# Optimization experiments

Measured on AMD Instinct MI355X. Metric: run time of the kernel, lower is better.

Reference implementation:

```python
import jax, jax.numpy as jnp
import numpy as np

B, T, C = 4, 2048, 1024
N_HEAD = 16
HEAD_DIM = C // N_HEAD


def setup_inputs() -> dict:
    key = jax.random.key(0)
    ks = jax.random.split(key, 5)
    scale = 0.02
    return {
        "x": jax.random.normal(ks[0], (B, T, C), dtype=jnp.float32),
        "w_attn": jax.random.normal(ks[1], (C, 3 * C), dtype=jnp.float32) * scale,
        "b_attn": jax.random.normal(ks[2], (3 * C,), dtype=jnp.float32) * scale,
        "w_proj": jax.random.normal(ks[3], (C, C), dtype=jnp.float32) * scale,
        "b_proj": jax.random.normal(ks[4], (C,), dtype=jnp.float32) * scale,
    }


def reference(x, w_attn, b_attn, w_proj, b_proj):
    Bq, Tq, Cq = x.shape
    qkv = x @ w_attn + b_attn  # [B, T, 3C]
    q, k, v = jnp.split(qkv, 3, axis=2)
    # [B, H, T, D]
    q = q.reshape(Bq, Tq, N_HEAD, HEAD_DIM).transpose(0, 2, 1, 3)
    k = k.reshape(Bq, Tq, N_HEAD, HEAD_DIM).transpose(0, 2, 1, 3)
    v = v.reshape(Bq, Tq, N_HEAD, HEAD_DIM).transpose(0, 2, 1, 3)
    att = jnp.einsum("bhqd,bhkd->bhqk", q, k) * (HEAD_DIM ** -0.5)
    causal = jnp.tril(jnp.ones((Tq, Tq), dtype=bool))
    att = jnp.where(causal[None, None, :, :], att, -jnp.inf)
    att = jax.nn.softmax(att, axis=-1)
    out = jnp.einsum("bhqk,bhkd->bhqd", att, v)  # [B, H, T, D]
    out = out.transpose(0, 2, 1, 3).reshape(Bq, Tq, Cq)
    return out @ w_proj + b_proj
```

## Files before the change

kernel.cpp:

```cpp
#include <hip/hip_runtime.h>
#include <hip/hip_bf16.h>

#define Bsz 4
#define Tsz 2048
#define Csz 1024
#define NH  16
#define HD  64
#define NT  (Bsz * Tsz)

typedef unsigned short u16;
typedef unsigned int   u32;
typedef u16   u16x8  __attribute__((ext_vector_type(8)));
typedef u16   u16x4  __attribute__((ext_vector_type(4)));
typedef short s16x8  __attribute__((ext_vector_type(8)));
typedef float f32x4  __attribute__((ext_vector_type(4)));

__device__ __forceinline__ float b2f(u16 u) {
    union { unsigned int i; float f; } x; x.i = ((unsigned int)u) << 16; return x.f;
}
__device__ __forceinline__ u16 f2b(float f) {
    unsigned int u = __float_as_uint(f);
    return (u16)((u + 0x7FFF + ((u >> 16) & 1)) >> 16);
}
__device__ __forceinline__ float ex2(float x) {
    float r; asm("v_exp_f32 %0, %1" : "=v"(r) : "v"(x)); return r;
}

__global__ __launch_bounds__(256)
void conv_f32_bf16(const float* __restrict__ in, u16* __restrict__ out, int n8)
{
    int t = blockIdx.x * 256 + threadIdx.x;
    if (t >= n8) return;
    const float4* p = reinterpret_cast<const float4*>(in) + (size_t)t * 2;
    float4 a = p[0], b = p[1];
    u16x8 w;
    w[0] = f2b(a.x); w[1] = f2b(a.y); w[2] = f2b(a.z); w[3] = f2b(a.w);
    w[4] = f2b(b.x); w[5] = f2b(b.y); w[6] = f2b(b.z); w[7] = f2b(b.w);
    *(reinterpret_cast<u16x8*>(out) + t) = w;
}

__global__ __launch_bounds__(256)
void transpose_conv(const float* __restrict__ in, u16* __restrict__ out, int K, int N)
{
    __shared__ float tile[32][33];
    const int n0 = blockIdx.x * 32, k0 = blockIdx.y * 32;
    const int tx = threadIdx.x & 31, ty = threadIdx.x >> 5;
#pragma unroll
    for (int j = 0; j < 4; ++j)
        tile[ty + j * 8][tx] = in[(size_t)(k0 + ty + j * 8) * N + n0 + tx];
    __syncthreads();
#pragma unroll
    for (int j = 0; j < 4; ++j)
        out[(size_t)(n0 + ty + j * 8) * K + k0 + tx] = f2b(tile[tx][ty + j * 8]);
}

template<typename OutT>
__global__ __launch_bounds__(256)
void gemm_bf16(const u16* __restrict__ A, const u16* __restrict__ Bt,
               const float* __restrict__ bias, OutT* __restrict__ C,
               int M, int N, int K)
{
    __shared__ u16 As[128 * 64];
    __shared__ u16 Bs[128 * 64];

    const int tid  = threadIdx.x;
    const int lane = tid & 63;
    const int wid  = tid >> 6;
    const int wr   = wid >> 1;
    const int wc   = wid & 1;
    const int g    = lane >> 4;
    const int rr   = lane & 15;

    const int n0 = blockIdx.x * 128;
    const int m0 = blockIdx.y * 128;

    f32x4 acc[4][4];
#pragma unroll
    for (int m = 0; m < 4; ++m)
#pragma unroll
        for (int n = 0; n < 4; ++n) acc[m][n] = (f32x4){0.f, 0.f, 0.f, 0.f};

    for (int k0 = 0; k0 < K; k0 += 64) {
        s16x8 va[4], vb[4];
#pragma unroll
        for (int p = 0; p < 4; ++p) {
            const int ci = p * 256 + tid;
            const int r = ci >> 3, s = ci & 7;
            va[p] = *reinterpret_cast<const s16x8*>(A  + (size_t)(m0 + r) * K + k0 + s * 8);
            vb[p] = *reinterpret_cast<const s16x8*>(Bt + (size_t)(n0 + r) * K + k0 + s * 8);
        }
        __syncthreads();
#pragma unroll
        for (int p = 0; p < 4; ++p) {
            const int ci = p * 256 + tid;
            const int r = ci >> 3, s = ci & 7;
            const int phys = r * 64 + ((s ^ (r & 7)) * 8);
            *reinterpret_cast<s16x8*>(&As[phys]) = va[p];
            *reinterpret_cast<s16x8*>(&Bs[phys]) = vb[p];
        }
        __syncthreads();

#pragma unroll
        for (int kk = 0; kk < 2; ++kk) {
            s16x8 af[4], bfr[4];
            const int s = kk * 4 + g;
#pragma unroll
            for (int m = 0; m < 4; ++m) {
                const int r = wr * 64 + m * 16 + rr;
                af[m] = *reinterpret_cast<const s16x8*>(&As[r * 64 + ((s ^ (r & 7)) * 8)]);
            }
#pragma unroll
            for (int n = 0; n < 4; ++n) {
                const int r = wc * 64 + n * 16 + rr;
                bfr[n] = *reinterpret_cast<const s16x8*>(&Bs[r * 64 + ((s ^ (r & 7)) * 8)]);
            }
#pragma unroll
            for (int m = 0; m < 4; ++m)
#pragma unroll
                for (int n = 0; n < 4; ++n)
                    acc[m][n] = __builtin_amdgcn_mfma_f32_16x16x32_bf16(
                        af[m], bfr[n], acc[m][n], 0, 0, 0);
        }
    }

#pragma unroll
    for (int m = 0; m < 4; ++m) {
#pragma unroll
        for (int n = 0; n < 4; ++n) {
            const int col = n0 + wc * 64 + n * 16 + rr;
            const float bv = bias[col];
#pragma unroll
            for (int j = 0; j < 4; ++j) {
                const int row = m0 + wr * 64 + m * 16 + g * 4 + j;
                const float v = acc[m][n][j] + bv;
                if constexpr (sizeof(OutT) == 2)
                    C[(size_t)row * N + col] = (OutT)f2b(v);
                else
                    C[(size_t)row * N + col] = (OutT)v;
            }
        }
    }
}

__global__ __launch_bounds__(256)
void attn_mfma(const u16* __restrict__ qkv, u16* __restrict__ out)
{
    __shared__ __align__(128) u16 Ks[64 * 64];
    __shared__ __align__(128) u16 Vt[64 * 64];
    __shared__ __align__(128) u16 Pl[4 * 2048];

    const int tid  = threadIdx.x;
    const int lane = tid & 63;
    const int wid  = tid >> 6;
    const int c    = lane & 15;
    const int g    = lane >> 4;

    const int bh = blockIdx.x;
    const int b  = bh >> 4;
    const int h  = bh & 15;
    const int t0 = ((int)gridDim.y - 1 - (int)blockIdx.y) * 128;
    const int qb0 = t0 + wid * 32;

    s16x8 qf[2][2];
#pragma unroll
    for (int m = 0; m < 2; ++m)
#pragma unroll
        for (int kk = 0; kk < 2; ++kk)
            qf[m][kk] = *reinterpret_cast<const s16x8*>(
                qkv + (size_t)(b * Tsz + qb0 + m * 16 + c) * (3 * Csz) + h * HD + kk * 32 + g * 8);

    f32x4 acco[2][4];
#pragma unroll
    for (int m = 0; m < 2; ++m)
#pragma unroll
        for (int dn = 0; dn < 4; ++dn) acco[m][dn] = (f32x4){0.f, 0.f, 0.f, 0.f};
    float mrun[8], lrun[8];
#pragma unroll
    for (int i = 0; i < 8; ++i) { mrun[i] = -1e30f; lrun[i] = 0.f; }

    const int skey = tid >> 3;
    const int sb   = tid & 7;
    const u32 pbyte = ((u32)(size_t)(&Pl[0])) + wid * 4096 + lane * 8;
    const float SC = 0.18033688f;

    for (int kt = 0; kt < t0 + 128; kt += 64) {
#pragma unroll
        for (int p = 0; p < 2; ++p) {
            const int key = skey + p * 32;
            const u16* gk = qkv + (size_t)(b * Tsz + kt + key) * (3 * Csz) + Csz + h * HD + sb * 8;
            u16x8 kv = *reinterpret_cast<const u16x8*>(gk);
            u16x8 vv = *reinterpret_cast<const u16x8*>(gk + Csz);
            *reinterpret_cast<u16x8*>(&Ks[key * 64 + ((sb ^ (key & 7)) * 8)]) = kv;
#pragma unroll
            for (int i = 0; i < 8; ++i) {
                const int d = sb * 8 + i;
                Vt[d * 64 + (key ^ (((i ^ sb) & 7) << 3))] = vv[i];
            }
        }
        __syncthreads();

        if (kt <= qb0 + 31) {
            f32x4 accS[2][4];
#pragma unroll
            for (int m = 0; m < 2; ++m)
#pragma unroll
                for (int n = 0; n < 4; ++n) accS[m][n] = (f32x4){0.f, 0.f, 0.f, 0.f};
#pragma unroll
            for (int kk = 0; kk < 2; ++kk) {
                s16x8 kf[4];
#pragma unroll
                for (int n = 0; n < 4; ++n) {
                    const int key = n * 16 + c;
                    kf[n] = *reinterpret_cast<const s16x8*>(
                        &Ks[key * 64 + (((kk * 4 + g) ^ (c & 7)) * 8)]);
                }
#pragma unroll
                for (int m = 0; m < 2; ++m)
#pragma unroll
                    for (int n = 0; n < 4; ++n)
                        accS[m][n] = __builtin_amdgcn_mfma_f32_16x16x32_bf16(
                            qf[m][kk], kf[n], accS[m][n], 0, 0, 0);
            }

            if (kt + 63 > qb0) {
#pragma unroll
                for (int m = 0; m < 2; ++m)
#pragma unroll
                    for (int n = 0; n < 4; ++n) {
                        const int kgl = kt + n * 16 + c;
#pragma unroll
                        for (int j = 0; j < 4; ++j) {
                            const int qg = qb0 + m * 16 + g * 4 + j;
                            if (kgl > qg) accS[m][n][j] = -1e30f;
                        }
                    }
            }

            float pm[8];
#pragma unroll
            for (int m = 0; m < 2; ++m)
#pragma unroll
                for (int j = 0; j < 4; ++j)
                    pm[m * 4 + j] = fmaxf(fmaxf(accS[m][0][j], accS[m][1][j]),
                                          fmaxf(accS[m][2][j], accS[m][3][j]));
#pragma unroll
            for (int msk = 1; msk < 16; msk <<= 1)
#pragma unroll
                for (int i = 0; i < 8; ++i)
                    pm[i] = fmaxf(pm[i], __shfl_xor(pm[i], msk));
            float cvec[8];
#pragma unroll
            for (int i = 0; i < 8; ++i) {
                const float mn = fmaxf(mrun[i], pm[i]);
                cvec[i] = ex2((mrun[i] - mn) * SC);
                mrun[i] = mn;
                lrun[i] *= cvec[i];
            }
#pragma unroll
            for (int m = 0; m < 2; ++m)
#pragma unroll
                for (int dn = 0; dn < 4; ++dn)
#pragma unroll
                    for (int j = 0; j < 4; ++j)
                        acco[m][dn][j] *= cvec[m * 4 + j];

#pragma unroll
            for (int m = 0; m < 2; ++m)
#pragma unroll
                for (int n = 0; n < 4; ++n) {
                    u16x4 pb;
#pragma unroll
                    for (int j = 0; j < 4; ++j) {
                        const float p = ex2((accS[m][n][j] - mrun[m * 4 + j]) * SC);
                        lrun[m * 4 + j] += p;
                        pb[j] = f2b(p);
                    }
                    const int slot = (n >> 1) * 32 + ((c >> 2) & 1) * 16
                                   + ((n & 1) * 2 + (c >> 3)) * 4 + (c & 3);
                    *reinterpret_cast<u16x4*>(&Pl[wid * 2048 + m * 1024 + slot * 16 + g * 4]) = pb;
                }
            asm volatile("s_waitcnt lgkmcnt(0)" ::: "memory");
            __builtin_amdgcn_sched_barrier(0);

            u16x4 t000, t001, t010, t011, t100, t101, t110, t111;
            asm volatile("ds_read_b64_tr_b16 %0, %1"             : "=v"(t000) : "v"(pbyte));
            asm volatile("ds_read_b64_tr_b16 %0, %1 offset:512"  : "=v"(t001) : "v"(pbyte));
            asm volatile("ds_read_b64_tr_b16 %0, %1 offset:1024" : "=v"(t010) : "v"(pbyte));
            asm volatile("ds_read_b64_tr_b16 %0, %1 offset:1536" : "=v"(t011) : "v"(pbyte));
            asm volatile("ds_read_b64_tr_b16 %0, %1 offset:2048" : "=v"(t100) : "v"(pbyte));
            asm volatile("ds_read_b64_tr_b16 %0, %1 offset:2560" : "=v"(t101) : "v"(pbyte));
            asm volatile("ds_read_b64_tr_b16 %0, %1 offset:3072" : "=v"(t110) : "v"(pbyte));
            asm volatile("ds_read_b64_tr_b16 %0, %1 offset:3584" : "=v"(t111) : "v"(pbyte));
            asm volatile("s_waitcnt lgkmcnt(0)" ::: "memory");
            __builtin_amdgcn_sched_barrier(0);

            s16x8 pa[2][2];
#pragma unroll
            for (int q = 0; q < 4; ++q) {
                pa[0][0][q] = (short)t000[q]; pa[0][0][q + 4] = (short)t001[q];
                pa[0][1][q] = (short)t010[q]; pa[0][1][q + 4] = (short)t011[q];
                pa[1][0][q] = (short)t100[q]; pa[1][0][q + 4] = (short)t101[q];
                pa[1][1][q] = (short)t110[q]; pa[1][1][q + 4] = (short)t111[q];
            }

#pragma unroll
            for (int kk = 0; kk < 2; ++kk) {
                s16x8 vf[4];
#pragma unroll
                for (int dn = 0; dn < 4; ++dn) {
                    const int d = dn * 16 + c;
                    const int swz = (c & 7) ^ ((dn * 2 + (c >> 3)) & 7);
                    vf[dn] = *reinterpret_cast<const s16x8*>(
                        &Vt[d * 64 + (((kk * 4 + g) ^ swz) * 8)]);
                }
#pragma unroll
                for (int m = 0; m < 2; ++m)
#pragma unroll
                    for (int dn = 0; dn < 4; ++dn)
                        acco[m][dn] = __builtin_amdgcn_mfma_f32_16x16x32_bf16(
                            pa[m][kk], vf[dn], acco[m][dn], 0, 0, 0);
            }
        }
        __syncthreads();
    }

#pragma unroll
    for (int msk = 1; msk < 16; msk <<= 1)
#pragma unroll
        for (int i = 0; i < 8; ++i)
            lrun[i] += __shfl_xor(lrun[i], msk);
    float inv[8];
#pragma unroll
    for (int i = 0; i < 8; ++i) inv[i] = 1.f / lrun[i];
#pragma unroll
    for (int m = 0; m < 2; ++m)
#pragma unroll
        for (int dn = 0; dn < 4; ++dn)
#pragma unroll
            for (int j = 0; j < 4; ++j) {
                const int q = qb0 + m * 16 + g * 4 + j;
                out[(size_t)(b * Tsz + q) * Csz + h * HD + dn * 16 + c] =
                    f2b(acco[m][dn][j] * inv[m * 4 + j]);
            }
}

extern "C" void kernel_launch(void* const* d_in, const int* in_sizes, int n_in,
                              void* d_out, int out_size, void* d_ws, size_t ws_size,
                              hipStream_t stream) {
    const float* x      = (const float*)d_in[0];
    const float* w_attn = (const float*)d_in[1];
    const float* b_attn = (const float*)d_in[2];
    const float* w_proj = (const float*)d_in[3];
    const float* b_proj = (const float*)d_in[4];
    float* out = (float*)d_out;

    char* w = (char*)d_ws;
    u16* qkv_bf = (u16*)w;  w += (size_t)NT * 3 * Csz * 2;
    u16* x_bf   = (u16*)w;  w += (size_t)NT * Csz * 2;
    u16* ao_bf  = (u16*)w;  w += (size_t)NT * Csz * 2;
    u16* wat    = (u16*)w;  w += (size_t)3 * Csz * Csz * 2;
    u16* wpt    = (u16*)w;

    conv_f32_bf16<<<(NT * Csz / 8 + 255) / 256, 256, 0, stream>>>(x, x_bf, NT * Csz / 8);
    transpose_conv<<<dim3(3 * Csz / 32, Csz / 32), 256, 0, stream>>>(w_attn, wat, Csz, 3 * Csz);
    transpose_conv<<<dim3(Csz / 32, Csz / 32), 256, 0, stream>>>(w_proj, wpt, Csz, Csz);

    gemm_bf16<u16><<<dim3(3 * Csz / 128, NT / 128), 256, 0, stream>>>(
        x_bf, wat, b_attn, qkv_bf, NT, 3 * Csz, Csz);

    attn_mfma<<<dim3(Bsz * NH, Tsz / 128), 256, 0, stream>>>(qkv_bf, ao_bf);

    gemm_bf16<float><<<dim3(Csz / 128, NT / 128), 256, 0, stream>>>(
        ao_bf, wpt, b_proj, out, NT, Csz, Csz);
}
```

Baseline: 306.6 us.

## Use direct global-to-LDS loads in GEMM and pair causal query tiles in attention

The GEMM now stages A and B tiles with global_load_lds straight into LDS instead of going through registers, which also drops the XOR swizzle (risking bank conflicts on the fragment reads). The attention kernel pairs query tile y with tile 15-y in each block to balance causal work, and halves the grid. It also folds the softmax scale into Q up front, skips rescaling the running max unless the max grows by more than a threshold (lazy rescale), and packs P to bf16 with v_cvt_pk_bf16_f32. Pre-scaling Q in bf16 adds a small rounding change, and the smaller grid may lower occupancy.

```diff
diff --git a/kernel.cpp b/kernel.cpp
--- a/kernel.cpp
+++ b/kernel.cpp
@@ -12,6 +12,7 @@
 typedef unsigned int   u32;
 typedef u16   u16x8  __attribute__((ext_vector_type(8)));
 typedef u16   u16x4  __attribute__((ext_vector_type(4)));
+typedef u32   u32x2  __attribute__((ext_vector_type(2)));
 typedef short s16x8  __attribute__((ext_vector_type(8)));
 typedef float f32x4  __attribute__((ext_vector_type(4)));
 
@@ -24,6 +25,14 @@
 }
 __device__ __forceinline__ float ex2(float x) {
     float r; asm("v_exp_f32 %0, %1" : "=v"(r) : "v"(x)); return r;
+}
+__device__ __forceinline__ u32 cvtpk(float lo, float hi) {
+    u32 r; asm("v_cvt_pk_bf16_f32 %0, %1, %2" : "=v"(r) : "v"(lo), "v"(hi)); return r;
+}
+__device__ __forceinline__ void gload16(const u16* g, u16* l) {
+    __builtin_amdgcn_global_load_lds(
+        (const __attribute__((address_space(1))) void*)g,
+        (__attribute__((address_space(3))) void*)l, 16, 0, 0);
 }
 
 __global__ __launch_bounds__(256)
@@ -70,6 +79,8 @@
     const int wc   = wid & 1;
     const int g    = lane >> 4;
     const int rr   = lane & 15;
+    const int srow = lane >> 3;
+    const int sslt = lane & 7;
 
     const int n0 = blockIdx.x * 128;
     const int m0 = blockIdx.y * 128;
@@ -81,22 +92,13 @@
         for (int n = 0; n < 4; ++n) acc[m][n] = (f32x4){0.f, 0.f, 0.f, 0.f};
 
     for (int k0 = 0; k0 < K; k0 += 64) {
-        s16x8 va[4], vb[4];
+        __syncthreads();
 #pragma unroll
         for (int p = 0; p < 4; ++p) {
-            const int ci = p * 256 + tid;
-            const int r = ci >> 3, s = ci & 7;
-            va[p] = *reinterpret_cast<const s16x8*>(A  + (size_t)(m0 + r) * K + k0 + s * 8);
-            vb[p] = *reinterpret_cast<const s16x8*>(Bt + (size_t)(n0 + r) * K + k0 + s * 8);
-        }
-        __syncthreads();
-#pragma unroll
-        for (int p = 0; p < 4; ++p) {
-            const int ci = p * 256 + tid;
-            const int r = ci >> 3, s = ci & 7;
-            const int phys = r * 64 + ((s ^ (r & 7)) * 8);
-            *reinterpret_cast<s16x8*>(&As[phys]) = va[p];
-            *reinterpret_cast<s16x8*>(&Bs[phys]) = vb[p];
+            const int q = p * 4 + wid;
+            const int r = q * 8 + srow;
+            gload16(A  + (size_t)(m0 + r) * K + k0 + sslt * 8, &As[q * 512]);
+            gload16(Bt + (size_t)(n0 + r) * K + k0 + sslt * 8, &Bs[q * 512]);
         }
         __syncthreads();
 
@@ -105,15 +107,13 @@
             s16x8 af[4], bfr[4];
             const int s = kk * 4 + g;
 #pragma unroll
-            for (int m = 0; m < 4; ++m) {
-                const int r = wr * 64 + m * 16 + rr;
-                af[m] = *reinterpret_cast<const s16x8*>(&As[r * 64 + ((s ^ (r & 7)) * 8)]);
-            }
-#pragma unroll
-            for (int n = 0; n < 4; ++n) {
-                const int r = wc * 64 + n * 16 + rr;
-                bfr[n] = *reinterpret_cast<const s16x8*>(&Bs[r * 64 + ((s ^ (r & 7)) * 8)]);
-            }
+            for (int m = 0; m < 4; ++m)
+                af[m] = *reinterpret_cast<const s16x8*>(
+                    &As[(wr * 64 + m * 16 + rr) * 64 + s * 8]);
+#pragma unroll
+            for (int n = 0; n < 4; ++n)
+                bfr[n] = *reinterpret_cast<const s16x8*>(
+                    &Bs[(wc * 64 + n * 16 + rr) * 64 + s * 8]);
 #pragma unroll
             for (int m = 0; m < 4; ++m)
 #pragma unroll
@@ -158,190 +158,208 @@
     const int bh = blockIdx.x;
     const int b  = bh >> 4;
     const int h  = bh & 15;
-    const int t0 = ((int)gridDim.y - 1 - (int)blockIdx.y) * 128;
-    const int qb0 = t0 + wid * 32;
-
-    s16x8 qf[2][2];
-#pragma unroll
-    for (int m = 0; m < 2; ++m)
-#pragma unroll
-        for (int kk = 0; kk < 2; ++kk)
-            qf[m][kk] = *reinterpret_cast<const s16x8*>(
-                qkv + (size_t)(b * Tsz + qb0 + m * 16 + c) * (3 * Csz) + h * HD + kk * 32 + g * 8);
-
-    f32x4 acco[2][4];
-#pragma unroll
-    for (int m = 0; m < 2; ++m)
-#pragma unroll
-        for (int dn = 0; dn < 4; ++dn) acco[m][dn] = (f32x4){0.f, 0.f, 0.f, 0.f};
-    float mrun[8], lrun[8];
-#pragma unroll
-    for (int i = 0; i < 8; ++i) { mrun[i] = -1e30f; lrun[i] = 0.f; }
-
     const int skey = tid >> 3;
     const int sb   = tid & 7;
     const u32 pbyte = ((u32)(size_t)(&Pl[0])) + wid * 4096 + lane * 8;
-    const float SC = 0.18033688f;
-
-    for (int kt = 0; kt < t0 + 128; kt += 64) {
-#pragma unroll
-        for (int p = 0; p < 2; ++p) {
-            const int key = skey + p * 32;
-            const u16* gk = qkv + (size_t)(b * Tsz + kt + key) * (3 * Csz) + Csz + h * HD + sb * 8;
-            u16x8 kv = *reinterpret_cast<const u16x8*>(gk);
-            u16x8 vv = *reinterpret_cast<const u16x8*>(gk + Csz);
-            *reinterpret_cast<u16x8*>(&Ks[key * 64 + ((sb ^ (key & 7)) * 8)]) = kv;
-#pragma unroll
-            for (int i = 0; i < 8; ++i) {
-                const int d = sb * 8 + i;
-                Vt[d * 64 + (key ^ (((i ^ sb) & 7) << 3))] = vv[i];
+    const float QSC = 0.18033688f;
+
+    for (int half = 0; half < 2; ++half) {
+        const int yt = half ? 15 - (int)blockIdx.y : (int)blockIdx.y;
+        const int t0 = yt * 128;
+        const int qb0 = t0 + wid * 32;
+
+        s16x8 qf[2][2];
+#pragma unroll
+        for (int m = 0; m < 2; ++m)
+#pragma unroll
+            for (int kk = 0; kk < 2; ++kk) {
+                u16x8 raw = *reinterpret_cast<const u16x8*>(
+                    qkv + (size_t)(b * Tsz + qb0 + m * 16 + c) * (3 * Csz)
+                        + h * HD + kk * 32 + g * 8);
+                s16x8 qv;
+#pragma unroll
+                for (int i = 0; i < 8; ++i) qv[i] = (short)f2b(b2f(raw[i]) * QSC);
+                qf[m][kk] = qv;
             }
+
+        f32x4 acco[2][4];
+#pragma unroll
+        for (int m = 0; m < 2; ++m)
+#pragma unroll
+            for (int dn = 0; dn < 4; ++dn) acco[m][dn] = (f32x4){0.f, 0.f, 0.f, 0.f};
+        float mrun[8], lrun[8];
+#pragma unroll
+        for (int i = 0; i < 8; ++i) { mrun[i] = -1e30f; lrun[i] = 0.f; }
+
+        for (int kt = 0; kt < t0 + 128; kt += 64) {
+#pragma unroll
+            for (int p = 0; p < 2; ++p) {
+                const int key = skey + p * 32;
+                const u16* gk = qkv + (size_t)(b * Tsz + kt + key) * (3 * Csz)
+                                + Csz + h * HD + sb * 8;
+                u16x8 kv = *reinterpret_cast<const u16x8*>(gk);
+                u16x8 vv = *reinterpret_cast<const u16x8*>(gk + Csz);
+                *reinterpret_cast<u16x8*>(&Ks[key * 64 + ((sb ^ (key & 7)) * 8)]) = kv;
+#pragma unroll
+                for (int i = 0; i < 8; ++i) {
+                    const int d = sb * 8 + i;
+                    Vt[d * 64 + (key ^ (((i ^ sb) & 7) << 3))] = vv[i];
+                }
+            }
+            __syncthreads();
+
+            if (kt <= qb0 + 31) {
+                f32x4 accS[2][4];
+#pragma unroll
+                for (int m = 0; m < 2; ++m)
+#pragma unroll
+                    for (int n = 0; n < 4; ++n) accS[m][n] = (f32x4){0.f, 0.f, 0.f, 0.f};
+#pragma unroll
+                for (int kk = 0; kk < 2; ++kk) {
+                    s16x8 kf[4];
+#pragma unroll
+                    for (int n = 0; n < 4; ++n) {
+                        const int key = n * 16 + c;
+                        kf[n] = *reinterpret_cast<const s16x8*>(
+                            &Ks[key * 64 + (((kk * 4 + g) ^ (c & 7)) * 8)]);
+                    }
+#pragma unroll
+                    for (int m = 0; m < 2; ++m)
+#pragma unroll
+                        for (int n = 0; n < 4; ++n)
+                            accS[m][n] = __builtin_amdgcn_mfma_f32_16x16x32_bf16(
+                                qf[m][kk], kf[n], accS[m][n], 0, 0, 0);
+                }
+
+                if (kt + 63 > qb0) {
+#pragma unroll
+                    for (int m = 0; m < 2; ++m)
+#pragma unroll
+                        for (int n = 0; n < 4; ++n) {
+                            const int kgl = kt + n * 16 + c;
+#pragma unroll
+                            for (int j = 0; j < 4; ++j) {
+                                const int qg = qb0 + m * 16 + g * 4 + j;
+                                if (kgl > qg) accS[m][n][j] = -1e30f;
+                            }
+                        }
+                }
+
+                float pm[8];
+#pragma unroll
+                for (int m = 0; m < 2; ++m)
+#pragma unroll
+                    for (int j = 0; j < 4; ++j)
+                        pm[m * 4 + j] = fmaxf(fmaxf(accS[m][0][j], accS[m][1][j]),
+                                              fmaxf(accS[m][2][j], accS[m][3][j]));
+#pragma unroll
+                for (int msk = 1; msk < 16; msk <<= 1)
+#pragma unroll
+                    for (int i = 0; i < 8; ++i)
+                        pm[i] = fmaxf(pm[i], __shfl_xor(pm[i], msk));
+
+                int need = 0;
+#pragma unroll
+                for (int i = 0; i < 8; ++i) need |= (pm[i] > mrun[i] + 8.f);
+                if (__any(need)) {
+                    float cvec[8];
+#pragma unroll
+                    for (int i = 0; i < 8; ++i) {
+                        const float mn = fmaxf(mrun[i], pm[i]);
+                        cvec[i] = ex2(mrun[i] - mn);
+                        mrun[i] = mn;
+                        lrun[i] *= cvec[i];
+                    }
+#pragma unroll
+                    for (int m = 0; m < 2; ++m)
+#pragma unroll
+                        for (int dn = 0; dn < 4; ++dn)
+#pragma unroll
+                            for (int j = 0; j < 4; ++j)
+                                acco[m][dn][j] *= cvec[m * 4 + j];
+                }
+
+#pragma unroll
+                for (int m = 0; m < 2; ++m)
+#pragma unroll
+                    for (int n = 0; n < 4; ++n) {
+                        float pv[4];
+#pragma unroll
+                        for (int j = 0; j < 4; ++j) {
+                            pv[j] = ex2(accS[m][n][j] - mrun[m * 4 + j]);
+                            lrun[m * 4 + j] += pv[j];
+                        }
+                        const u32 w0 = cvtpk(pv[0], pv[1]);
+                        const u32 w1 = cvtpk(pv[2], pv[3]);
+                        const int slot = (n >> 1) * 32 + ((c >> 2) & 1) * 16
+                                       + ((n & 1) * 2 + (c >> 3)) * 4 + (c & 3);
+                        *reinterpret_cast<u32x2*>(
+                            &Pl[wid * 2048 + m * 1024 + slot * 16 + g * 4]) = (u32x2){w0, w1};
+                    }
+                asm volatile("s_waitcnt lgkmcnt(0)" ::: "memory");
+                __builtin_amdgcn_sched_barrier(0);
+
+                u16x4 t000, t001, t010, t011, t100, t101, t110, t111;
+                asm volatile("ds_read_b64_tr_b16 %0, %1"             : "=v"(t000) : "v"(pbyte));
+                asm volatile("ds_read_b64_tr_b16 %0, %1 offset:512"  : "=v"(t001) : "v"(pbyte));
+                asm volatile("ds_read_b64_tr_b16 %0, %1 offset:1024" : "=v"(t010) : "v"(pbyte));
+                asm volatile("ds_read_b64_tr_b16 %0, %1 offset:1536" : "=v"(t011) : "v"(pbyte));
+                asm volatile("ds_read_b64_tr_b16 %0, %1 offset:2048" : "=v"(t100) : "v"(pbyte));
+                asm volatile("ds_read_b64_tr_b16 %0, %1 offset:2560" : "=v"(t101) : "v"(pbyte));
+                asm volatile("ds_read_b64_tr_b16 %0, %1 offset:3072" : "=v"(t110) : "v"(pbyte));
+                asm volatile("ds_read_b64_tr_b16 %0, %1 offset:3584" : "=v"(t111) : "v"(pbyte));
+                asm volatile("s_waitcnt lgkmcnt(0)" ::: "memory");
+                __builtin_amdgcn_sched_barrier(0);
+
+                s16x8 pa[2][2];
+#pragma unroll
+                for (int q = 0; q < 4; ++q) {
+                    pa[0][0][q] = (short)t000[q]; pa[0][0][q + 4] = (short)t001[q];
+                    pa[0][1][q] = (short)t010[q]; pa[0][1][q + 4] = (short)t011[q];
+                    pa[1][0][q] = (short)t100[q]; pa[1][0][q + 4] = (short)t101[q];
+                    pa[1][1][q] = (short)t110[q]; pa[1][1][q + 4] = (short)t111[q];
+                }
+
+#pragma unroll
+                for (int kk = 0; kk < 2; ++kk) {
+                    s16x8 vf[4];
+#pragma unroll
+                    for (int dn = 0; dn < 4; ++dn) {
+                        const int d = dn * 16 + c;
+                        const int swz = (c & 7) ^ ((dn * 2 + (c >> 3)) & 7);
+                        vf[dn] = *reinterpret_cast<const s16x8*>(
+                            &Vt[d * 64 + (((kk * 4 + g) ^ swz) * 8)]);
+                    }
+#pragma unroll
+                    for (int m = 0; m < 2; ++m)
+#pragma unroll
+                        for (int dn = 0; dn < 4; ++dn)
+                            acco[m][dn] = __builtin_amdgcn_mfma_f32_16x16x32_bf16(
+                                pa[m][kk], vf[dn], acco[m][dn], 0, 0, 0);
+                }
+            }
+            __syncthreads();
         }
-        __syncthreads();
-
-        if (kt <= qb0 + 31) {
-            f32x4 accS[2][4];
-#pragma unroll
-            for (int m = 0; m < 2; ++m)
-#pragma unroll
-                for (int n = 0; n < 4; ++n) accS[m][n] = (f32x4){0.f, 0.f, 0.f, 0.f};
-#pragma unroll
-            for (int kk = 0; kk < 2; ++kk) {
-                s16x8 kf[4];
-#pragma unroll
-                for (int n = 0; n < 4; ++n) {
-                    const int key = n * 16 + c;
-                    kf[n] = *reinterpret_cast<const s16x8*>(
-                        &Ks[key * 64 + (((kk * 4 + g) ^ (c & 7)) * 8)]);
-                }
-#pragma unroll
-                for (int m = 0; m < 2; ++m)
-#pragma unroll
-                    for (int n = 0; n < 4; ++n)
-                        accS[m][n] = __builtin_amdgcn_mfma_f32_16x16x32_bf16(
-                            qf[m][kk], kf[n], accS[m][n], 0, 0, 0);
-            }
-
-            if (kt + 63 > qb0) {
-#pragma unroll
-                for (int m = 0; m < 2; ++m)
-#pragma unroll
-                    for (int n = 0; n < 4; ++n) {
-                        const int kgl = kt + n * 16 + c;
-#pragma unroll
-                        for (int j = 0; j < 4; ++j) {
-                            const int qg = qb0 + m * 16 + g * 4 + j;
-                            if (kgl > qg) accS[m][n][j] = -1e30f;
-                        }
-                    }
-            }
-
-            float pm[8];
-#pragma unroll
-            for (int m = 0; m < 2; ++m)
-#pragma unroll
-                for (int j = 0; j < 4; ++j)
-                    pm[m * 4 + j] = fmaxf(fmaxf(accS[m][0][j], accS[m][1][j]),
-                                          fmaxf(accS[m][2][j], accS[m][3][j]));
-#pragma unroll
-            for (int msk = 1; msk < 16; msk <<= 1)
-#pragma unroll
-                for (int i = 0; i < 8; ++i)
-                    pm[i] = fmaxf(pm[i], __shfl_xor(pm[i], msk));
-            float cvec[8];
-#pragma unroll
-            for (int i = 0; i < 8; ++i) {
-                const float mn = fmaxf(mrun[i], pm[i]);
-                cvec[i] = ex2((mrun[i] - mn) * SC);
-                mrun[i] = mn;
-                lrun[i] *= cvec[i];
-            }
-#pragma unroll
-            for (int m = 0; m < 2; ++m)
-#pragma unroll
-                for (int dn = 0; dn < 4; ++dn)
-#pragma unroll
-                    for (int j = 0; j < 4; ++j)
-                        acco[m][dn][j] *= cvec[m * 4 + j];
-
-#pragma unroll
-            for (int m = 0; m < 2; ++m)
-#pragma unroll
-                for (int n = 0; n < 4; ++n) {
-                    u16x4 pb;
-#pragma unroll
-                    for (int j = 0; j < 4; ++j) {
-                        const float p = ex2((accS[m][n][j] - mrun[m * 4 + j]) * SC);
-                        lrun[m * 4 + j] += p;
-                        pb[j] = f2b(p);
-                    }
-                    const int slot = (n >> 1) * 32 + ((c >> 2) & 1) * 16
-                                   + ((n & 1) * 2 + (c >> 3)) * 4 + (c & 3);
-                    *reinterpret_cast<u16x4*>(&Pl[wid * 2048 + m * 1024 + slot * 16 + g * 4]) = pb;
-                }
-            asm volatile("s_waitcnt lgkmcnt(0)" ::: "memory");
-            __builtin_amdgcn_sched_barrier(0);
-
-            u16x4 t000, t001, t010, t011, t100, t101, t110, t111;
-            asm volatile("ds_read_b64_tr_b16 %0, %1"             : "=v"(t000) : "v"(pbyte));
-            asm volatile("ds_read_b64_tr_b16 %0, %1 offset:512"  : "=v"(t001) : "v"(pbyte));
-            asm volatile("ds_read_b64_tr_b16 %0, %1 offset:1024" : "=v"(t010) : "v"(pbyte));
-            asm volatile("ds_read_b64_tr_b16 %0, %1 offset:1536" : "=v"(t011) : "v"(pbyte));
-            asm volatile("ds_read_b64_tr_b16 %0, %1 offset:2048" : "=v"(t100) : "v"(pbyte));
-            asm volatile("ds_read_b64_tr_b16 %0, %1 offset:2560" : "=v"(t101) : "v"(pbyte));
-            asm volatile("ds_read_b64_tr_b16 %0, %1 offset:3072" : "=v"(t110) : "v"(pbyte));
-            asm volatile("ds_read_b64_tr_b16 %0, %1 offset:3584" : "=v"(t111) : "v"(pbyte));
-            asm volatile("s_waitcnt lgkmcnt(0)" ::: "memory");
-            __builtin_amdgcn_sched_barrier(0);
-
-            s16x8 pa[2][2];
-#pragma unroll
-            for (int q = 0; q < 4; ++q) {
-                pa[0][0][q] = (short)t000[q]; pa[0][0][q + 4] = (short)t001[q];
-                pa[0][1][q] = (short)t010[q]; pa[0][1][q + 4] = (short)t011[q];
-                pa[1][0][q] = (short)t100[q]; pa[1][0][q + 4] = (short)t101[q];
-                pa[1][1][q] = (short)t110[q]; pa[1][1][q + 4] = (short)t111[q];
-            }
-
-#pragma unroll
-            for (int kk = 0; kk < 2; ++kk) {
-                s16x8 vf[4];
-#pragma unroll
-                for (int dn = 0; dn < 4; ++dn) {
-                    const int d = dn * 16 + c;
-                    const int swz = (c & 7) ^ ((dn * 2 + (c >> 3)) & 7);
-                    vf[dn] = *reinterpret_cast<const s16x8*>(
-                        &Vt[d * 64 + (((kk * 4 + g) ^ swz) * 8)]);
-                }
-#pragma unroll
-                for (int m = 0; m < 2; ++m)
-#pragma unroll
-                    for (int dn = 0; dn < 4; ++dn)
-                        acco[m][dn] = __builtin_amdgcn_mfma_f32_16x16x32_bf16(
-                            pa[m][kk], vf[dn], acco[m][dn], 0, 0, 0);
-            }
-        }
-        __syncthreads();
+
+#pragma unroll
+        for (int msk = 1; msk < 16; msk <<= 1)
+#pragma unroll
+            for (int i = 0; i < 8; ++i)
+                lrun[i] += __shfl_xor(lrun[i], msk);
+        float inv[8];
+#pragma unroll
+        for (int i = 0; i < 8; ++i) inv[i] = 1.f / lrun[i];
+#pragma unroll
+        for (int m = 0; m < 2; ++m)
+#pragma unroll
+            for (int dn = 0; dn < 4; ++dn)
+#pragma unroll
+                for (int j = 0; j < 4; ++j) {
+                    const int q = qb0 + m * 16 + g * 4 + j;
+                    out[(size_t)(b * Tsz + q) * Csz + h * HD + dn * 16 + c] =
+                        f2b(acco[m][dn][j] * inv[m * 4 + j]);
+                }
     }
-
-#pragma unroll
-    for (int msk = 1; msk < 16; msk <<= 1)
-#pragma unroll
-        for (int i = 0; i < 8; ++i)
-            lrun[i] += __shfl_xor(lrun[i], msk);
-    float inv[8];
-#pragma unroll
-    for (int i = 0; i < 8; ++i) inv[i] = 1.f / lrun[i];
-#pragma unroll
-    for (int m = 0; m < 2; ++m)
-#pragma unroll
-        for (int dn = 0; dn < 4; ++dn)
-#pragma unroll
-            for (int j = 0; j < 4; ++j) {
-                const int q = qb0 + m * 16 + g * 4 + j;
-                out[(size_t)(b * Tsz + q) * Csz + h * HD + dn * 16 + c] =
-                    f2b(acco[m][dn][j] * inv[m * 4 + j]);
-            }
 }
 
 extern "C" void kernel_launch(void* const* d_in, const int* in_sizes, int n_in,
@@ -368,7 +386,7 @@
     gemm_bf16<u16><<<dim3(3 * Csz / 128, NT / 128), 256, 0, stream>>>(
         x_bf, wat, b_attn, qkv_bf, NT, 3 * Csz, Csz);
 
-    attn_mfma<<<dim3(Bsz * NH, Tsz / 128), 256, 0, stream>>>(qkv_bf, ao_bf);
+    attn_mfma<<<dim3(Bsz * NH, 8), 256, 0, stream>>>(qkv_bf, ao_bf);
 
     gemm_bf16<float><<<dim3(Csz / 128, NT / 128), 256, 0, stream>>>(
         ao_bf, wpt, b_proj, out, NT, Csz, Csz);
```

Result: faster. 299.9 us (-2.2%).
